# Kernel optimization log

Hardware: AMD Instinct MI355X
Metric: run time of the kernel (lower is better)

The kernel has to match this reference:

```python
import jax, jax.numpy as jnp
import numpy as np

N_NODES = 50000
N_EDGES = 800000
DIM_IN, DIM_H, DIM_OUT = 128, 128, 64


def _init_linear(key, fan_in, fan_out):
    # kaiming-uniform-ish init, matches torch Linear scale
    lim = 1.0 / np.sqrt(fan_in)
    return jax.random.uniform(key, (fan_in, fan_out), jnp.float32, -lim, lim)


def setup_inputs() -> dict:
    key = jax.random.key(0)
    ks = jax.random.split(key, 12)
    x = jax.random.normal(ks[0], (N_NODES, DIM_IN), jnp.float32)
    edge_index = jax.random.randint(ks[1], (2, N_EDGES), 0, N_NODES, jnp.int32)
    dims = [(DIM_IN, DIM_H), (DIM_H, DIM_H), (DIM_H, DIM_OUT)]
    inp = {"x": x, "edge_index": edge_index}
    for i, (fi, fo) in enumerate(dims):
        inp[f"Wl{i}"] = _init_linear(ks[2 + 3 * i], fi, fo)   # neighbor transform
        inp[f"Wr{i}"] = _init_linear(ks[3 + 3 * i], fi, fo)   # root transform
        inp[f"b{i}"] = jnp.zeros((fo,), jnp.float32)
    return inp


def _sage_layer(x, src, dst, Wl, Wr, b):
    # mean aggregation of neighbor messages x[src] at destination nodes
    msg = x[src]                                              # [E, d]
    agg = jax.ops.segment_sum(msg, dst, num_segments=N_NODES)  # [N, d]
    cnt = jax.ops.segment_sum(jnp.ones((src.shape[0],), x.dtype), dst,
                              num_segments=N_NODES)
    mean = agg / jnp.maximum(cnt, 1.0)[:, None]               # isolated nodes -> 0
    return mean @ Wl + b + x @ Wr                              # SAGEConv


def reference(x, edge_index, Wl0, Wr0, b0, Wl1, Wr1, b1, Wl2, Wr2, b2):
    src, dst = edge_index[0], edge_index[1]
    layers = [(Wl0, Wr0, b0), (Wl1, Wr1, b1), (Wl2, Wr2, b2)]
    h = x
    for i, (Wl, Wr, b) in enumerate(layers):
        h = _sage_layer(h, src, dst, Wl, Wr, b)
        if i != len(layers) - 1:
            h = jax.nn.relu(h)  # dropout p=0.2 is identity in eval mode
    return jax.nn.log_softmax(h, axis=1), h
```

## Files before the change

### kernel.cpp

```cpp
#include <hip/hip_runtime.h>

#define N_NODES 50000
#define N_EDGES 800000
#define SCAN_BLOCKS 196
#define WIN 6250
#define PLANE 1600000

typedef __attribute__((ext_vector_type(8))) short short8;
typedef __attribute__((ext_vector_type(4))) float f32x4;
typedef unsigned short ushort_t;
typedef unsigned int uint_t;

__device__ inline ushort_t f2bf(float f) {
    union { float f; uint_t u; } v; v.f = f;
    uint_t u = v.u;
    u += 0x7fffu + ((u >> 16) & 1u);
    return (ushort_t)(u >> 16);
}
__device__ inline float bflo(uint_t v) { return __uint_as_float(v << 16); }
__device__ inline float bfhi(uint_t v) { return __uint_as_float(v & 0xffff0000u); }
__device__ inline float bf2f(ushort_t v) { return __uint_as_float((uint_t)v << 16); }

#define ACC8(V) { a[0] += bflo((V).x); a[1] += bfhi((V).x); \
                  a[2] += bflo((V).y); a[3] += bfhi((V).y); \
                  a[4] += bflo((V).z); a[5] += bfhi((V).z); \
                  a[6] += bflo((V).w); a[7] += bfhi((V).w); }

__global__ void count_edges_mp(const int* __restrict__ ei, int* __restrict__ cnt) {
    int g = blockIdx.x & 7;
    int nb = gridDim.x >> 3;
    int bi = blockIdx.x >> 3;
    int lo = g * WIN;
    for (int e = bi * 256 + threadIdx.x; e < N_EDGES; e += nb * 256) {
        int d = ei[N_EDGES + e];
        if ((unsigned)(d - lo) < WIN) atomicAdd(&cnt[d], 1);
    }
}

__global__ void fill_csr_mp(const int* __restrict__ ei, int* __restrict__ cursor,
                            int* __restrict__ csr_src) {
    int g = blockIdx.x & 7;
    int nb = gridDim.x >> 3;
    int bi = blockIdx.x >> 3;
    int lo = g * WIN;
    for (int e = bi * 256 + threadIdx.x; e < N_EDGES; e += nb * 256) {
        int d = ei[N_EDGES + e];
        if ((unsigned)(d - lo) < WIN) {
            int p = atomicAdd(&cursor[d], 1);
            csr_src[p] = ei[e];
        }
    }
}

__global__ void block_sums(const int* __restrict__ cnt, int* __restrict__ bsum) {
    int i = blockIdx.x * 256 + threadIdx.x;
    int v = (i < N_NODES) ? cnt[i] : 0;
    for (int off = 32; off; off >>= 1) v += __shfl_down(v, off, 64);
    __shared__ int s[4];
    if ((threadIdx.x & 63) == 0) s[threadIdx.x >> 6] = v;
    __syncthreads();
    if (threadIdx.x == 0) bsum[blockIdx.x] = s[0] + s[1] + s[2] + s[3];
}

__global__ void scan_bsums(const int* __restrict__ bsum, int* __restrict__ bprefix,
                           int* __restrict__ rowstart) {
    __shared__ int s[256];
    int t = threadIdx.x;
    int v = (t < SCAN_BLOCKS) ? bsum[t] : 0;
    s[t] = v;
    __syncthreads();
    for (int off = 1; off < 256; off <<= 1) {
        int add = (t >= off) ? s[t - off] : 0;
        __syncthreads();
        s[t] += add;
        __syncthreads();
    }
    bprefix[t] = s[t] - v;
    if (t == 0) rowstart[N_NODES] = N_EDGES;
}

__global__ void apply_scan(const int* __restrict__ cnt, const int* __restrict__ bprefix,
                           int* __restrict__ rowstart, int* __restrict__ cursor) {
    __shared__ int s[256];
    int t = threadIdx.x;
    int i = blockIdx.x * 256 + t;
    int v = (i < N_NODES) ? cnt[i] : 0;
    s[t] = v;
    __syncthreads();
    for (int off = 1; off < 256; off <<= 1) {
        int add = (t >= off) ? s[t - off] : 0;
        __syncthreads();
        s[t] += add;
        __syncthreads();
    }
    int excl = s[t] - v + bprefix[blockIdx.x];
    if (i < N_NODES) { rowstart[i] = excl; cursor[i] = excl; }
}

__global__ void cvt_bf16_pl(const float* __restrict__ in, ushort_t* __restrict__ out) {
    int i = blockIdx.x * 256 + threadIdx.x;
    if (i >= 1600000) return;
    int d0 = (i & 31) * 4;
    int node = i >> 5;
    float4 v = ((const float4*)in)[i];
    ushort4 o;
    o.x = f2bf(v.x); o.y = f2bf(v.y); o.z = f2bf(v.z); o.w = f2bf(v.w);
    int p = d0 >> 5, dd = d0 & 31;
    *(ushort4*)(out + ((size_t)p * 50000 + node) * 32 + dd) = o;
}

__global__ void pack_all(const float* __restrict__ Wl0, const float* __restrict__ Wr0,
                         const float* __restrict__ Wl1, const float* __restrict__ Wr1,
                         const float* __restrict__ Wl2, const float* __restrict__ Wr2,
                         ushort_t* __restrict__ pk0, ushort_t* __restrict__ pk1,
                         ushort_t* __restrict__ pkz) {
    int gi = blockIdx.x * 256 + threadIdx.x;
    const float* Wl; const float* Wr; ushort_t* dst; int idx; bool zr = false;
    if (gi < 32768)       { Wl = Wl0; Wr = Wr0; dst = pk0; idx = gi; }
    else if (gi < 65536)  { Wl = Wl1; Wr = Wr1; dst = pk1; idx = gi - 32768; }
    else if (gi < 81920)  { Wl = Wl2; Wr = Wr2; dst = pkz; idx = gi - 65536; zr = true; }
    else return;
    int j = idx & 7, l = (idx >> 3) & 63, t = (idx >> 9) & 7, ks = idx >> 12;
    int n = t * 16 + (l & 15);
    int k = ks * 32 + (l >> 4) * 8 + j;
    float w;
    if (zr) w = (n < 64) ? Wl[k * 64 + n] : Wr[k * 64 + (n - 64)];
    else    w = (k < 128) ? Wl[k * 128 + n] : Wr[(k - 128) * 128 + n];
    dst[idx] = f2bf(w);
}

__global__ __launch_bounds__(256) void agg_pl(
    const ushort_t* __restrict__ feat_pl,
    const int* __restrict__ rowstart,
    const int* __restrict__ csr_src,
    ushort_t* __restrict__ mean_pl) {
    int role = blockIdx.x & 7;
    int wi   = blockIdx.x >> 3;
    int s    = role >> 1, half = role & 1;
    int lane = threadIdx.x & 63, wave = threadIdx.x >> 6;
    int sub = lane >> 4, sl = lane & 15, gb = sub << 4;
    const uint_t* pbase = (const uint_t*)feat_pl + (size_t)s * (PLANE / 2);
    uint_t* mbase = (uint_t*)mean_pl + (size_t)s * (PLANE / 2);
    int nodeBase = half * 25000 + wi * 64 + wave * 16;
    int nodeLim  = (half + 1) * 25000;

    for (int p = 0; p < 4; ++p) {
        int node = nodeBase + p * 4 + sub;
        bool nv = node < nodeLim;
        int s0 = 0, s1 = 0;
        if (nv) { s0 = rowstart[node]; s1 = rowstart[node + 1]; }
        float a0 = 0.f, a1 = 0.f;

        int pos = s0;
        while (__any(pos < s1)) {
            int m = min(16, s1 - pos);
            int idxr = (sl < m) ? __builtin_nontemporal_load(&csr_src[pos + sl]) : 0;
            int mm = max(m, 0);
            mm = max(mm, __shfl_xor(mm, 16, 64));
            mm = max(mm, __shfl_xor(mm, 32, 64));
            for (int j = 0; j < mm; j += 8) {
                int  sidx[8];
                bool vld[8];
                #pragma unroll
                for (int k = 0; k < 8; ++k) {
                    int q = __shfl(idxr, (gb + j + k) & 63, 64);
                    vld[k]  = (j + k < m);
                    sidx[k] = vld[k] ? q : 0;
                }
                uint_t V[8];
                #pragma unroll
                for (int k = 0; k < 8; ++k)
                    V[k] = pbase[(size_t)sidx[k] * 16 + sl];
                #pragma unroll
                for (int k = 0; k < 8; ++k)
                    if (vld[k]) { a0 += bflo(V[k]); a1 += bfhi(V[k]); }
            }
            pos += 16;
        }
        if (nv) {
            float inv = 1.0f / fmaxf((float)(s1 - s0), 1.0f);
            uint_t packed = (uint_t)f2bf(a0 * inv) | ((uint_t)f2bf(a1 * inv) << 16);
            __builtin_nontemporal_store(packed, &mbase[(size_t)node * 16 + sl]);
        }
    }
}

__global__ __launch_bounds__(256) void gemm_pl(
    const ushort_t* __restrict__ mean_pl, const ushort_t* __restrict__ root_pl,
    const ushort_t* __restrict__ Bpk, const float* __restrict__ bias,
    ushort_t* __restrict__ out_pl) {
    __shared__ ushort_t bsh[32768];
    {
        const uint4* src = (const uint4*)Bpk;
        uint4* dst = (uint4*)bsh;
        for (int i = threadIdx.x; i < 4096; i += 256) dst[i] = src[i];
    }
    __syncthreads();

    int lane = threadIdx.x & 63;
    int wave = threadIdx.x >> 6;
    int row16 = lane & 15;
    int quad = lane >> 4;
    int rowBase = blockIdx.x * 64 + wave * 16;
    int arow = min(rowBase + row16, N_NODES - 1);
    const short8* bp = (const short8*)bsh + lane;

    f32x4 acc[8];
    #pragma unroll
    for (int t = 0; t < 8; ++t) { f32x4 z = {0.f, 0.f, 0.f, 0.f}; acc[t] = z; }

    #pragma unroll
    for (int ks = 0; ks < 8; ++ks) {
        const ushort_t* ab = (ks < 4)
            ? (mean_pl + ((size_t)ks * 50000 + arow) * 32 + quad * 8)
            : (root_pl + ((size_t)(ks - 4) * 50000 + arow) * 32 + quad * 8);
        short8 afrag = *(const short8*)ab;
        #pragma unroll
        for (int t = 0; t < 8; ++t) {
            short8 bfrag = bp[(ks * 8 + t) * 64];
            acc[t] = __builtin_amdgcn_mfma_f32_16x16x32_bf16(afrag, bfrag, acc[t], 0, 0, 0);
        }
    }

    #pragma unroll
    for (int t = 0; t < 8; ++t) {
        int col = t * 16 + row16;
        float bv = bias[col];
        int pl = col >> 5, dd = col & 31;
        #pragma unroll
        for (int r = 0; r < 4; ++r) {
            int row = rowBase + quad * 4 + r;
            if (row < N_NODES) {
                float v = fmaxf(acc[t][r] + bv, 0.f);
                out_pl[((size_t)pl * 50000 + row) * 32 + dd] = f2bf(v);
            }
        }
    }
}

__global__ __launch_bounds__(256) void gemm_zr_pl(
    const ushort_t* __restrict__ h_pl, const ushort_t* __restrict__ Bpk,
    const float* __restrict__ bias,
    ushort_t* __restrict__ z_bf, float* __restrict__ r_f32) {
    __shared__ ushort_t bsh[16384];
    {
        const uint4* src = (const uint4*)Bpk;
        uint4* dst = (uint4*)bsh;
        for (int i = threadIdx.x; i < 2048; i += 256) dst[i] = src[i];
    }
    __syncthreads();

    int lane = threadIdx.x & 63;
    int wave = threadIdx.x >> 6;
    int row16 = lane & 15;
    int quad = lane >> 4;
    int rowBase = blockIdx.x * 64 + wave * 16;
    int arow = min(rowBase + row16, N_NODES - 1);
    const short8* bp = (const short8*)bsh + lane;

    f32x4 acc[8];
    #pragma unroll
    for (int t = 0; t < 8; ++t) { f32x4 z = {0.f, 0.f, 0.f, 0.f}; acc[t] = z; }

    #pragma unroll
    for (int ks = 0; ks < 4; ++ks) {
        short8 afrag = *(const short8*)(h_pl + ((size_t)ks * 50000 + arow) * 32 + quad * 8);
        #pragma unroll
        for (int t = 0; t < 8; ++t) {
            short8 bfrag = bp[(ks * 8 + t) * 64];
            acc[t] = __builtin_amdgcn_mfma_f32_16x16x32_bf16(afrag, bfrag, acc[t], 0, 0, 0);
        }
    }

    #pragma unroll
    for (int t = 0; t < 8; ++t) {
        int col = t * 16 + row16;
        #pragma unroll
        for (int r = 0; r < 4; ++r) {
            int row = rowBase + quad * 4 + r;
            if (row < N_NODES) {
                if (col < 64) {
                    z_bf[(size_t)row * 64 + col] = f2bf(acc[t][r]);
                } else {
                    r_f32[(size_t)row * 64 + (col - 64)] = acc[t][r] + bias[col - 64];
                }
            }
        }
    }
}

__global__ __launch_bounds__(256) void final_agg_softmax2(
    const ushort_t* __restrict__ z_bf, const float* __restrict__ r_f32,
    const int* __restrict__ rowstart, const int* __restrict__ csr_src,
    float* __restrict__ out) {
    int lane = threadIdx.x & 63;
    int wave = threadIdx.x >> 6;
    int sub = lane >> 3;
    int sl  = lane & 7;
    int gb  = sub << 3;
    int node = blockIdx.x * 32 + wave * 8 + sub;
    int s0 = 0, s1 = 0;
    if (node < N_NODES) { s0 = rowstart[node]; s1 = rowstart[node + 1]; }

    float a[8];
    #pragma unroll
    for (int k = 0; k < 8; ++k) a[k] = 0.f;
    const uint_t* zb = (const uint_t*)z_bf;

    int pos = s0;
    while (__any(pos < s1)) {
        int m = min(8, s1 - pos);
        int idxr = (sl < m) ? csr_src[pos + sl] : 0;
        int  sidx[8];
        bool vld[8];
        #pragma unroll
        for (int k = 0; k < 8; ++k) {
            int q = __shfl(idxr, (gb + k) & 63, 64);
            vld[k]  = (k < m);
            sidx[k] = vld[k] ? q : 0;
        }
        uint4 V[8];
        #pragma unroll
        for (int k = 0; k < 8; ++k)
            V[k] = *(const uint4*)(zb + (size_t)sidx[k] * 32 + (sl << 2));
        #pragma unroll
        for (int k = 0; k < 8; ++k)
            if (vld[k]) { ACC8(V[k]); }
        pos += 8;
    }
    if (node >= N_NODES) return;

    float inv = 1.0f / fmaxf((float)(s1 - s0), 1.0f);
    const float4* rr = (const float4*)(r_f32 + (size_t)node * 64 + sl * 8);
    float4 rA = rr[0], rB = rr[1];
    float h[8];
    h[0] = a[0] * inv + rA.x; h[1] = a[1] * inv + rA.y;
    h[2] = a[2] * inv + rA.z; h[3] = a[3] * inv + rA.w;
    h[4] = a[4] * inv + rB.x; h[5] = a[5] * inv + rB.y;
    h[6] = a[6] * inv + rB.z; h[7] = a[7] * inv + rB.w;

    float mx = fmaxf(fmaxf(fmaxf(h[0], h[1]), fmaxf(h[2], h[3])),
                     fmaxf(fmaxf(h[4], h[5]), fmaxf(h[6], h[7])));
    mx = fmaxf(mx, __shfl_xor(mx, 1, 64));
    mx = fmaxf(mx, __shfl_xor(mx, 2, 64));
    mx = fmaxf(mx, __shfl_xor(mx, 4, 64));
    float s = 0.f;
    #pragma unroll
    for (int k = 0; k < 8; ++k) s += expf(h[k] - mx);
    s += __shfl_xor(s, 1, 64);
    s += __shfl_xor(s, 2, 64);
    s += __shfl_xor(s, 4, 64);
    float lse = mx + logf(s);

    size_t o1 = (size_t)node * 64 + sl * 8;
    size_t o2 = (size_t)N_NODES * 64 + o1;
    *(float4*)(out + o1)     = make_float4(h[0] - lse, h[1] - lse, h[2] - lse, h[3] - lse);
    *(float4*)(out + o1 + 4) = make_float4(h[4] - lse, h[5] - lse, h[6] - lse, h[7] - lse);
    *(float4*)(out + o2)     = make_float4(h[0], h[1], h[2], h[3]);
    *(float4*)(out + o2 + 4) = make_float4(h[4], h[5], h[6], h[7]);
}

extern "C" void kernel_launch(void* const* d_in, const int* in_sizes, int n_in,
                              void* d_out, int out_size, void* d_ws, size_t ws_size,
                              hipStream_t stream) {
    const float* x  = (const float*)d_in[0];
    const int* ei   = (const int*)d_in[1];
    const float* Wl0 = (const float*)d_in[2];
    const float* Wr0 = (const float*)d_in[3];
    const float* b0  = (const float*)d_in[4];
    const float* Wl1 = (const float*)d_in[5];
    const float* Wr1 = (const float*)d_in[6];
    const float* b1  = (const float*)d_in[7];
    const float* Wl2 = (const float*)d_in[8];
    const float* Wr2 = (const float*)d_in[9];
    const float* b2  = (const float*)d_in[10];
    float* out = (float*)d_out;

    char* ws = (char*)d_ws;
    int* cnt      = (int*)(ws + 0x000000);
    int* rowstart = (int*)(ws + 0x040000);
    int* cursor   = (int*)(ws + 0x080000);
    int* bsum     = (int*)(ws + 0x0C0000);
    int* bprefix  = (int*)(ws + 0x0C1000);
    int* csr_src  = (int*)(ws + 0x100000);
    ushort_t* pk0 = (ushort_t*)(ws + 0x420000);
    ushort_t* pk1 = (ushort_t*)(ws + 0x440000);
    ushort_t* pkz = (ushort_t*)(ws + 0x460000);
    ushort_t* x_pl    = (ushort_t*)(ws + 0x0500000);
    ushort_t* mean_pl = (ushort_t*)(ws + 0x1200000);
    ushort_t* h_pl    = (ushort_t*)(ws + 0x1F00000);
    ushort_t* h2_pl   = (ushort_t*)(ws + 0x2C00000);
    ushort_t* z_bf    = (ushort_t*)(ws + 0x3900000);
    float*    r_f32   = (float*)  (ws + 0x4000000);

    pack_all<<<320, 256, 0, stream>>>(Wl0, Wr0, Wl1, Wr1, Wl2, Wr2, pk0, pk1, pkz);

    hipMemsetAsync(cnt, 0, N_NODES * sizeof(int), stream);
    count_edges_mp<<<1024, 256, 0, stream>>>(ei, cnt);
    block_sums<<<SCAN_BLOCKS, 256, 0, stream>>>(cnt, bsum);
    scan_bsums<<<1, 256, 0, stream>>>(bsum, bprefix, rowstart);
    apply_scan<<<SCAN_BLOCKS, 256, 0, stream>>>(cnt, bprefix, rowstart, cursor);
    fill_csr_mp<<<1024, 256, 0, stream>>>(ei, cursor, csr_src);

    cvt_bf16_pl<<<6250, 256, 0, stream>>>(x, x_pl);

    agg_pl<<<3128, 256, 0, stream>>>(x_pl, rowstart, csr_src, mean_pl);
    gemm_pl<<<782, 256, 0, stream>>>(mean_pl, x_pl, pk0, b0, h_pl);

    agg_pl<<<3128, 256, 0, stream>>>(h_pl, rowstart, csr_src, mean_pl);
    gemm_pl<<<782, 256, 0, stream>>>(mean_pl, h_pl, pk1, b1, h2_pl);

    gemm_zr_pl<<<782, 256, 0, stream>>>(h2_pl, pkz, b2, z_bf, r_f32);
    final_agg_softmax2<<<1563, 256, 0, stream>>>(z_bf, r_f32, rowstart, csr_src, out);
}
```

Measured before the change: 337.5 us.

## Edge-balanced segmented aggregation with degree scaling moved into GEMM

Aggregation kernels now walk contiguous edge ranges that are split into equal-sized chunks by binary search over rowstart, so each 4-lane group processes a balanced amount of edges and flushes per-node sums. Degree normalization moves into the GEMM epilogue through a precomputed inverse-degree array, and the final layer aggregation is split into a segmented sum followed by a separate softmax kernel. This targets load imbalance from skewed degrees and wave divergence in the old per-node loops. The cost is an extra partition kernel, an extra fp32 sum buffer and softmax pass, and a serial per-lane edge loop with less memory-level parallelism per thread.

```diff
diff --git a/kernel.cpp b/kernel.cpp
--- a/kernel.cpp
+++ b/kernel.cpp
@@ -5,6 +5,8 @@
 #define SCAN_BLOCKS 196
 #define WIN 6250
 #define PLANE 1600000
+#define AGG_B 120
+#define GHALF (AGG_B * 64)
 
 typedef __attribute__((ext_vector_type(8))) short short8;
 typedef __attribute__((ext_vector_type(4))) float f32x4;
@@ -19,7 +21,6 @@
 }
 __device__ inline float bflo(uint_t v) { return __uint_as_float(v << 16); }
 __device__ inline float bfhi(uint_t v) { return __uint_as_float(v & 0xffff0000u); }
-__device__ inline float bf2f(ushort_t v) { return __uint_as_float((uint_t)v << 16); }
 
 #define ACC8(V) { a[0] += bflo((V).x); a[1] += bfhi((V).x); \
                   a[2] += bflo((V).y); a[3] += bfhi((V).y); \
@@ -80,7 +81,8 @@
 }
 
 __global__ void apply_scan(const int* __restrict__ cnt, const int* __restrict__ bprefix,
-                           int* __restrict__ rowstart, int* __restrict__ cursor) {
+                           int* __restrict__ rowstart, int* __restrict__ cursor,
+                           float* __restrict__ invd) {
     __shared__ int s[256];
     int t = threadIdx.x;
     int i = blockIdx.x * 256 + t;
@@ -94,7 +96,28 @@
         __syncthreads();
     }
     int excl = s[t] - v + bprefix[blockIdx.x];
-    if (i < N_NODES) { rowstart[i] = excl; cursor[i] = excl; }
+    if (i < N_NODES) {
+        rowstart[i] = excl; cursor[i] = excl;
+        invd[i] = 1.0f / fmaxf((float)v, 1.0f);
+    }
+}
+
+__global__ void part_groups(const int* __restrict__ rowstart, int* __restrict__ gs) {
+    int gid = blockIdx.x * 256 + threadIdx.x;
+    if (gid >= 2 * (GHALF + 1)) return;
+    int h = gid / (GHALF + 1), g = gid % (GHALF + 1);
+    int nlo = h * 25000, nhi = nlo + 25000;
+    if (g == 0)      { gs[gid] = nlo; return; }
+    if (g == GHALF)  { gs[gid] = nhi; return; }
+    int base = rowstart[nlo];
+    int tot = rowstart[nhi] - base;
+    long target = (long)base + (long)g * tot / GHALF;
+    int lo = nlo, hi = nhi;
+    while (hi - lo > 1) {
+        int mid = (lo + hi) >> 1;
+        if ((long)rowstart[mid] >= target) hi = mid; else lo = mid;
+    }
+    gs[gid] = hi;
 }
 
 __global__ void cvt_bf16_pl(const float* __restrict__ in, ushort_t* __restrict__ out) {
@@ -129,65 +152,54 @@
     dst[idx] = f2bf(w);
 }
 
-__global__ __launch_bounds__(256) void agg_pl(
+#define AGG_FLUSH() { \
+    uint_t r0, r1, r2, r3; \
+    asm("v_cvt_pk_bf16_f32 %0, %1, %2" : "=v"(r0) : "v"(a[0]), "v"(a[1])); \
+    asm("v_cvt_pk_bf16_f32 %0, %1, %2" : "=v"(r1) : "v"(a[2]), "v"(a[3])); \
+    asm("v_cvt_pk_bf16_f32 %0, %1, %2" : "=v"(r2) : "v"(a[4]), "v"(a[5])); \
+    asm("v_cvt_pk_bf16_f32 %0, %1, %2" : "=v"(r3) : "v"(a[6]), "v"(a[7])); \
+    uint4 ov; ov.x = r0; ov.y = r1; ov.z = r2; ov.w = r3; \
+    ((uint4*)mb)[(size_t)node * 4 + sl] = ov; \
+    a[0]=0.f;a[1]=0.f;a[2]=0.f;a[3]=0.f;a[4]=0.f;a[5]=0.f;a[6]=0.f;a[7]=0.f; \
+    ++node; sEnd = rowstart[node + 1]; }
+
+__global__ __launch_bounds__(256) void agg_seg(
     const ushort_t* __restrict__ feat_pl,
     const int* __restrict__ rowstart,
     const int* __restrict__ csr_src,
-    ushort_t* __restrict__ mean_pl) {
+    const int* __restrict__ gs,
+    ushort_t* __restrict__ sum_pl) {
     int role = blockIdx.x & 7;
-    int wi   = blockIdx.x >> 3;
-    int s    = role >> 1, half = role & 1;
+    int bi   = blockIdx.x >> 3;
+    int s = role >> 1, h = role & 1;
     int lane = threadIdx.x & 63, wave = threadIdx.x >> 6;
-    int sub = lane >> 4, sl = lane & 15, gb = sub << 4;
-    const uint_t* pbase = (const uint_t*)feat_pl + (size_t)s * (PLANE / 2);
-    uint_t* mbase = (uint_t*)mean_pl + (size_t)s * (PLANE / 2);
-    int nodeBase = half * 25000 + wi * 64 + wave * 16;
-    int nodeLim  = (half + 1) * 25000;
-
-    for (int p = 0; p < 4; ++p) {
-        int node = nodeBase + p * 4 + sub;
-        bool nv = node < nodeLim;
-        int s0 = 0, s1 = 0;
-        if (nv) { s0 = rowstart[node]; s1 = rowstart[node + 1]; }
-        float a0 = 0.f, a1 = 0.f;
-
-        int pos = s0;
-        while (__any(pos < s1)) {
-            int m = min(16, s1 - pos);
-            int idxr = (sl < m) ? __builtin_nontemporal_load(&csr_src[pos + sl]) : 0;
-            int mm = max(m, 0);
-            mm = max(mm, __shfl_xor(mm, 16, 64));
-            mm = max(mm, __shfl_xor(mm, 32, 64));
-            for (int j = 0; j < mm; j += 8) {
-                int  sidx[8];
-                bool vld[8];
-                #pragma unroll
-                for (int k = 0; k < 8; ++k) {
-                    int q = __shfl(idxr, (gb + j + k) & 63, 64);
-                    vld[k]  = (j + k < m);
-                    sidx[k] = vld[k] ? q : 0;
-                }
-                uint_t V[8];
-                #pragma unroll
-                for (int k = 0; k < 8; ++k)
-                    V[k] = pbase[(size_t)sidx[k] * 16 + sl];
-                #pragma unroll
-                for (int k = 0; k < 8; ++k)
-                    if (vld[k]) { a0 += bflo(V[k]); a1 += bfhi(V[k]); }
-            }
-            pos += 16;
-        }
-        if (nv) {
-            float inv = 1.0f / fmaxf((float)(s1 - s0), 1.0f);
-            uint_t packed = (uint_t)f2bf(a0 * inv) | ((uint_t)f2bf(a1 * inv) << 16);
-            __builtin_nontemporal_store(packed, &mbase[(size_t)node * 16 + sl]);
-        }
-    }
+    int grp = lane >> 2, sl = lane & 3;
+    int gl = (bi * 4 + wave) * 16 + grp;
+    const int* gsh = gs + h * (GHALF + 1);
+    int n0 = gsh[gl], n1 = gsh[gl + 1];
+    if (n0 >= n1) return;
+    const uint4* pb = (const uint4*)((const uint_t*)feat_pl + (size_t)s * (PLANE / 2));
+    uint_t* mb = (uint_t*)sum_pl + (size_t)s * (PLANE / 2);
+
+    float a[8] = {0.f,0.f,0.f,0.f,0.f,0.f,0.f,0.f};
+    int e = rowstart[n0];
+    int eEnd = rowstart[n1];
+    int node = n0;
+    int sEnd = rowstart[n0 + 1];
+
+    for (; e < eEnd; ++e) {
+        while (e >= sEnd) { AGG_FLUSH(); }
+        int idx = csr_src[e];
+        uint4 v = pb[(size_t)idx * 4 + sl];
+        ACC8(v);
+    }
+    while (node < n1) { AGG_FLUSH(); }
 }
 
 __global__ __launch_bounds__(256) void gemm_pl(
-    const ushort_t* __restrict__ mean_pl, const ushort_t* __restrict__ root_pl,
+    const ushort_t* __restrict__ sum_pl, const ushort_t* __restrict__ root_pl,
     const ushort_t* __restrict__ Bpk, const float* __restrict__ bias,
+    const float* __restrict__ invd,
     ushort_t* __restrict__ out_pl) {
     __shared__ ushort_t bsh[32768];
     {
@@ -210,11 +222,25 @@
     for (int t = 0; t < 8; ++t) { f32x4 z = {0.f, 0.f, 0.f, 0.f}; acc[t] = z; }
 
     #pragma unroll
-    for (int ks = 0; ks < 8; ++ks) {
-        const ushort_t* ab = (ks < 4)
-            ? (mean_pl + ((size_t)ks * 50000 + arow) * 32 + quad * 8)
-            : (root_pl + ((size_t)(ks - 4) * 50000 + arow) * 32 + quad * 8);
-        short8 afrag = *(const short8*)ab;
+    for (int ks = 0; ks < 4; ++ks) {
+        short8 afrag = *(const short8*)(sum_pl + ((size_t)ks * 50000 + arow) * 32 + quad * 8);
+        #pragma unroll
+        for (int t = 0; t < 8; ++t) {
+            short8 bfrag = bp[(ks * 8 + t) * 64];
+            acc[t] = __builtin_amdgcn_mfma_f32_16x16x32_bf16(afrag, bfrag, acc[t], 0, 0, 0);
+        }
+    }
+    {
+        float4 iv = *(const float4*)(invd + rowBase + quad * 4);
+        #pragma unroll
+        for (int t = 0; t < 8; ++t) {
+            acc[t][0] *= iv.x; acc[t][1] *= iv.y;
+            acc[t][2] *= iv.z; acc[t][3] *= iv.w;
+        }
+    }
+    #pragma unroll
+    for (int ks = 4; ks < 8; ++ks) {
+        short8 afrag = *(const short8*)(root_pl + ((size_t)(ks - 4) * 50000 + arow) * 32 + quad * 8);
         #pragma unroll
         for (int t = 0; t < 8; ++t) {
             short8 bfrag = bp[(ks * 8 + t) * 64];
@@ -241,7 +267,7 @@
 __global__ __launch_bounds__(256) void gemm_zr_pl(
     const ushort_t* __restrict__ h_pl, const ushort_t* __restrict__ Bpk,
     const float* __restrict__ bias,
-    ushort_t* __restrict__ z_bf, float* __restrict__ r_f32) {
+    ushort_t* __restrict__ z_pl, float* __restrict__ r_f32) {
     __shared__ ushort_t bsh[16384];
     {
         const uint4* src = (const uint4*)Bpk;
@@ -280,7 +306,7 @@
             int row = rowBase + quad * 4 + r;
             if (row < N_NODES) {
                 if (col < 64) {
-                    z_bf[(size_t)row * 64 + col] = f2bf(acc[t][r]);
+                    z_pl[((size_t)(col >> 5) * 50000 + row) * 32 + (col & 31)] = f2bf(acc[t][r]);
                 } else {
                     r_f32[(size_t)row * 64 + (col - 64)] = acc[t][r] + bias[col - 64];
                 }
@@ -289,75 +315,65 @@
     }
 }
 
-__global__ __launch_bounds__(256) void final_agg_softmax2(
-    const ushort_t* __restrict__ z_bf, const float* __restrict__ r_f32,
-    const int* __restrict__ rowstart, const int* __restrict__ csr_src,
-    float* __restrict__ out) {
-    int lane = threadIdx.x & 63;
-    int wave = threadIdx.x >> 6;
-    int sub = lane >> 3;
-    int sl  = lane & 7;
-    int gb  = sub << 3;
-    int node = blockIdx.x * 32 + wave * 8 + sub;
-    int s0 = 0, s1 = 0;
-    if (node < N_NODES) { s0 = rowstart[node]; s1 = rowstart[node + 1]; }
-
-    float a[8];
-    #pragma unroll
-    for (int k = 0; k < 8; ++k) a[k] = 0.f;
-    const uint_t* zb = (const uint_t*)z_bf;
-
-    int pos = s0;
-    while (__any(pos < s1)) {
-        int m = min(8, s1 - pos);
-        int idxr = (sl < m) ? csr_src[pos + sl] : 0;
-        int  sidx[8];
-        bool vld[8];
-        #pragma unroll
-        for (int k = 0; k < 8; ++k) {
-            int q = __shfl(idxr, (gb + k) & 63, 64);
-            vld[k]  = (k < m);
-            sidx[k] = vld[k] ? q : 0;
-        }
-        uint4 V[8];
-        #pragma unroll
-        for (int k = 0; k < 8; ++k)
-            V[k] = *(const uint4*)(zb + (size_t)sidx[k] * 32 + (sl << 2));
-        #pragma unroll
-        for (int k = 0; k < 8; ++k)
-            if (vld[k]) { ACC8(V[k]); }
-        pos += 8;
-    }
+__global__ __launch_bounds__(256) void fin_seg(
+    const ushort_t* __restrict__ z_pl,
+    const int* __restrict__ rowstart,
+    const int* __restrict__ csr_src,
+    const int* __restrict__ gs,
+    float* __restrict__ fsum) {
+    int role = blockIdx.x & 3;
+    int bi   = blockIdx.x >> 2;
+    int s = role >> 1, h = role & 1;
+    int lane = threadIdx.x & 63, wave = threadIdx.x >> 6;
+    int grp = lane >> 2, sl = lane & 3;
+    int gl = (bi * 4 + wave) * 16 + grp;
+    const int* gsh = gs + h * (GHALF + 1);
+    int n0 = gsh[gl], n1 = gsh[gl + 1];
+    if (n0 >= n1) return;
+    const uint4* pb = (const uint4*)((const uint_t*)z_pl + (size_t)s * (PLANE / 2));
+    float* fb = fsum + (size_t)s * PLANE;
+
+    float a[8] = {0.f,0.f,0.f,0.f,0.f,0.f,0.f,0.f};
+    int e = rowstart[n0];
+    int eEnd = rowstart[n1];
+    int node = n0;
+    int sEnd = rowstart[n0 + 1];
+
+#define FIN_FLUSH() { \
+    *(float4*)(fb + (size_t)node * 32 + sl * 8)     = make_float4(a[0], a[1], a[2], a[3]); \
+    *(float4*)(fb + (size_t)node * 32 + sl * 8 + 4) = make_float4(a[4], a[5], a[6], a[7]); \
+    a[0]=0.f;a[1]=0.f;a[2]=0.f;a[3]=0.f;a[4]=0.f;a[5]=0.f;a[6]=0.f;a[7]=0.f; \
+    ++node; sEnd = rowstart[node + 1]; }
+
+    for (; e < eEnd; ++e) {
+        while (e >= sEnd) { FIN_FLUSH(); }
+        int idx = csr_src[e];
+        uint4 v = pb[(size_t)idx * 4 + sl];
+        ACC8(v);
+    }
+    while (node < n1) { FIN_FLUSH(); }
+#undef FIN_FLUSH
+}
+
+__global__ __launch_bounds__(256) void softmax_fin(
+    const float* __restrict__ fsum, const float* __restrict__ r_f32,
+    const float* __restrict__ invd, float* __restrict__ out) {
+    int node = blockIdx.x * 4 + (threadIdx.x >> 6);
+    int d = threadIdx.x & 63;
     if (node >= N_NODES) return;
-
-    float inv = 1.0f / fmaxf((float)(s1 - s0), 1.0f);
-    const float4* rr = (const float4*)(r_f32 + (size_t)node * 64 + sl * 8);
-    float4 rA = rr[0], rB = rr[1];
-    float h[8];
-    h[0] = a[0] * inv + rA.x; h[1] = a[1] * inv + rA.y;
-    h[2] = a[2] * inv + rA.z; h[3] = a[3] * inv + rA.w;
-    h[4] = a[4] * inv + rB.x; h[5] = a[5] * inv + rB.y;
-    h[6] = a[6] * inv + rB.z; h[7] = a[7] * inv + rB.w;
-
-    float mx = fmaxf(fmaxf(fmaxf(h[0], h[1]), fmaxf(h[2], h[3])),
-                     fmaxf(fmaxf(h[4], h[5]), fmaxf(h[6], h[7])));
-    mx = fmaxf(mx, __shfl_xor(mx, 1, 64));
-    mx = fmaxf(mx, __shfl_xor(mx, 2, 64));
-    mx = fmaxf(mx, __shfl_xor(mx, 4, 64));
-    float s = 0.f;
-    #pragma unroll
-    for (int k = 0; k < 8; ++k) s += expf(h[k] - mx);
-    s += __shfl_xor(s, 1, 64);
-    s += __shfl_xor(s, 2, 64);
-    s += __shfl_xor(s, 4, 64);
-    float lse = mx + logf(s);
-
-    size_t o1 = (size_t)node * 64 + sl * 8;
-    size_t o2 = (size_t)N_NODES * 64 + o1;
-    *(float4*)(out + o1)     = make_float4(h[0] - lse, h[1] - lse, h[2] - lse, h[3] - lse);
-    *(float4*)(out + o1 + 4) = make_float4(h[4] - lse, h[5] - lse, h[6] - lse, h[7] - lse);
-    *(float4*)(out + o2)     = make_float4(h[0], h[1], h[2], h[3]);
-    *(float4*)(out + o2 + 4) = make_float4(h[4], h[5], h[6], h[7]);
+    float inv = invd[node];
+    float sum = fsum[(size_t)(d >> 5) * PLANE + (size_t)node * 32 + (d & 31)];
+    float h = sum * inv + r_f32[(size_t)node * 64 + d];
+
+    float mx = h;
+    for (int off = 32; off; off >>= 1) mx = fmaxf(mx, __shfl_xor(mx, off, 64));
+    float e = expf(h - mx);
+    float ssum = e;
+    for (int off = 32; off; off >>= 1) ssum += __shfl_xor(ssum, off, 64);
+    float lse = mx + logf(ssum);
+
+    out[(size_t)node * 64 + d] = h - lse;
+    out[(size_t)N_NODES * 64 + (size_t)node * 64 + d] = h;
 }
 
 extern "C" void kernel_launch(void* const* d_in, const int* in_sizes, int n_in,
@@ -382,16 +398,19 @@
     int* cursor   = (int*)(ws + 0x080000);
     int* bsum     = (int*)(ws + 0x0C0000);
     int* bprefix  = (int*)(ws + 0x0C1000);
+    int* gs       = (int*)(ws + 0x0C2000);
     int* csr_src  = (int*)(ws + 0x100000);
     ushort_t* pk0 = (ushort_t*)(ws + 0x420000);
     ushort_t* pk1 = (ushort_t*)(ws + 0x440000);
     ushort_t* pkz = (ushort_t*)(ws + 0x460000);
+    float* invd   = (float*)(ws + 0x480000);
     ushort_t* x_pl    = (ushort_t*)(ws + 0x0500000);
-    ushort_t* mean_pl = (ushort_t*)(ws + 0x1200000);
+    ushort_t* sum_pl  = (ushort_t*)(ws + 0x1200000);
     ushort_t* h_pl    = (ushort_t*)(ws + 0x1F00000);
     ushort_t* h2_pl   = (ushort_t*)(ws + 0x2C00000);
-    ushort_t* z_bf    = (ushort_t*)(ws + 0x3900000);
+    ushort_t* z_pl    = (ushort_t*)(ws + 0x3900000);
     float*    r_f32   = (float*)  (ws + 0x4000000);
+    float*    fsum    = (float*)  (ws + 0x4D00000);
 
     pack_all<<<320, 256, 0, stream>>>(Wl0, Wr0, Wl1, Wr1, Wl2, Wr2, pk0, pk1, pkz);
 
@@ -399,17 +418,19 @@
     count_edges_mp<<<1024, 256, 0, stream>>>(ei, cnt);
     block_sums<<<SCAN_BLOCKS, 256, 0, stream>>>(cnt, bsum);
     scan_bsums<<<1, 256, 0, stream>>>(bsum, bprefix, rowstart);
-    apply_scan<<<SCAN_BLOCKS, 256, 0, stream>>>(cnt, bprefix, rowstart, cursor);
+    apply_scan<<<SCAN_BLOCKS, 256, 0, stream>>>(cnt, bprefix, rowstart, cursor, invd);
     fill_csr_mp<<<1024, 256, 0, stream>>>(ei, cursor, csr_src);
+    part_groups<<<61, 256, 0, stream>>>(rowstart, gs);
 
     cvt_bf16_pl<<<6250, 256, 0, stream>>>(x, x_pl);
 
-    agg_pl<<<3128, 256, 0, stream>>>(x_pl, rowstart, csr_src, mean_pl);
-    gemm_pl<<<782, 256, 0, stream>>>(mean_pl, x_pl, pk0, b0, h_pl);
-
-    agg_pl<<<3128, 256, 0, stream>>>(h_pl, rowstart, csr_src, mean_pl);
-    gemm_pl<<<782, 256, 0, stream>>>(mean_pl, h_pl, pk1, b1, h2_pl);
-
-    gemm_zr_pl<<<782, 256, 0, stream>>>(h2_pl, pkz, b2, z_bf, r_f32);
-    final_agg_softmax2<<<1563, 256, 0, stream>>>(z_bf, r_f32, rowstart, csr_src, out);
-}
+    agg_seg<<<8 * AGG_B, 256, 0, stream>>>(x_pl, rowstart, csr_src, gs, sum_pl);
+    gemm_pl<<<782, 256, 0, stream>>>(sum_pl, x_pl, pk0, b0, invd, h_pl);
+
+    agg_seg<<<8 * AGG_B, 256, 0, stream>>>(h_pl, rowstart, csr_src, gs, sum_pl);
+    gemm_pl<<<782, 256, 0, stream>>>(sum_pl, h_pl, pk1, b1, invd, h2_pl);
+
+    gemm_zr_pl<<<782, 256, 0, stream>>>(h2_pl, pkz, b2, z_pl, r_f32);
+    fin_seg<<<4 * AGG_B, 256, 0, stream>>>(z_pl, rowstart, csr_src, gs, fsum);
+    softmax_fin<<<12500, 256, 0, stream>>>(fsum, r_f32, invd, out);
+}
```

After: 420.3 us. +24.5%, slower.
